# Kernel optimization log

Measured on AMD Instinct MI355X. Metric: run time of the kernel, lower is better.

Reference implementation:

```python
import jax, jax.numpy as jnp
import numpy as np

INITIAL_RADIUS = 1.0  # init_kwargs: initial_radius > 0 -> distance-softmax branch


def reference(xyz, sparse_xyz, sparse_flow, resol_factor, K):
    # xyz: [B,3,N], sparse_xyz: [B,3,M], sparse_flow: [B,3,M]
    q = jnp.transpose(xyz, (0, 2, 1))            # [B,N,3]
    p = jnp.transpose(sparse_xyz, (0, 2, 1))     # [B,M,3]
    flow = jnp.transpose(sparse_flow, (0, 2, 1))  # [B,M,3]

    sigma = INITIAL_RADIUS * resol_factor
    qs = q / sigma
    ps = p / sigma

    # pairwise Euclidean distances [B,N,M]
    sq = (jnp.sum(qs * qs, -1)[:, :, None]
          + jnp.sum(ps * ps, -1)[:, None, :]
          - 2.0 * jnp.einsum('bnc,bmc->bnm', qs, ps))
    dist = jnp.sqrt(jnp.maximum(sq, 1e-12))

    # K nearest: smallest distances
    neg_d, idx = jax.lax.top_k(-dist, K)          # [B,N,K]
    K_dist = -neg_d                               # [B,N,K]

    # gather flow of the K neighbors: [B,N,K,3]
    grouped_flow = jnp.take_along_axis(flow[:, None, :, :], idx[..., None], axis=2)

    # softmax over -distance along K, weighted sum
    K_w = jax.nn.softmax(-K_dist, axis=2)         # [B,N,K]
    dense_flow = jnp.sum(K_w[..., None] * grouped_flow, axis=2)  # [B,N,3]

    return jnp.transpose(dense_flow, (0, 2, 1))   # [B,3,N]


def setup_inputs() -> dict:
    key = jax.random.key(0)
    k1, k2, k3 = jax.random.split(key, 3)
    B, N, M = 4, 16384, 4096
    return {
        'xyz': jax.random.normal(k1, (B, 3, N), dtype=jnp.float32),
        'sparse_xyz': jax.random.normal(k2, (B, 3, M), dtype=jnp.float32),
        'sparse_flow': jax.random.normal(k3, (B, 3, M), dtype=jnp.float32),
        'resol_factor': 1,
        'K': 5,
    }
```

## Files before the change

### kernel.cpp

```cpp
#include <hip/hip_runtime.h>
#include <math.h>
#include <stdint.h>


#define KNN 5
#define SLICES 8
#define BLOCK (SLICES * 64)
#define GRP_SHIFT 8

typedef unsigned int u32;

__device__ __forceinline__ float get_inv_sigma(const int* __restrict__ rf) {
    const int ri = rf[0];
    const float sigma = (ri >= 1 && ri <= 1000000) ? (float)ri : __int_as_float(ri);
    return 1.0f / sigma;
}

__global__ __launch_bounds__(256)
void prep_kernel(const float* __restrict__ sxyz, const int* __restrict__ rf,
                 float4* __restrict__ pts, int M, int total) {
    const int t = blockIdx.x * 256 + threadIdx.x;
    if (t >= total) return;
    const float inv = get_inv_sigma(rf);
    const int b = t / M, m = t - b * M;
    const float* sb = sxyz + (size_t)b * 3 * M;
    const float x = sb[m] * inv;
    const float y = sb[M + m] * inv;
    const float z = sb[2 * M + m] * inv;
    pts[t] = make_float4(x, y, z, fmaf(x, x, fmaf(y, y, z * z)));
}

#define CE_FULL(k, ki, c, ci)                          \
    {                                                  \
        const bool sw = (c) < (k);                     \
        const float vmn = fminf(k, c);                 \
        const float vmx = fmaxf(k, c);                 \
        const u32 nki = sw ? (ci) : (ki);              \
        const u32 nci = sw ? (ki) : (ci);              \
        (k) = vmn; (c) = vmx; (ki) = nki; (ci) = nci;  \
    }
#define CE_LAST(k, ki, c, ci)                          \
    {                                                  \
        const bool sw = (c) < (k);                     \
        (ki) = sw ? (ci) : (ki);                       \
        (k) = fminf(k, c);                             \
    }

template <bool USE_PTS>
__global__ __launch_bounds__(BLOCK, 8)
void knn_kernel(const float* __restrict__ xyz,
                const float* __restrict__ sxyz,
                const float* __restrict__ sflow,
                const int* __restrict__ rf,
                const float4* __restrict__ pts,
                float* __restrict__ out,
                int N, int M) {
    __shared__ float sval_d[SLICES * KNN * 64];
    __shared__ u32   sval_i[SLICES * KNN * 64];

    const int tid  = threadIdx.x;
    const int lane = tid & 63;
    const int wid  = tid >> 6;
    const int swid = __builtin_amdgcn_readfirstlane(wid);
    const int b    = blockIdx.x >> GRP_SHIFT;
    const int grp  = blockIdx.x & ((1 << GRP_SHIFT) - 1);
    const int n    = grp * 64 + lane;

    const float inv = get_inv_sigma(rf);
    const float* qb = xyz + (size_t)b * 3 * N;
    const float qx = qb[n] * inv;
    const float qy = qb[N + n] * inv;
    const float qz = qb[2 * N + n] * inv;
    const float qq = fmaf(qx, qx, fmaf(qy, qy, qz * qz));

    const int CH = M / SLICES;
    const int j0 = swid * CH;

    float e0 = 1e30f, e1 = 1e30f, e2 = 1e30f, e3 = 1e30f, e4 = 1e30f;
    u32   i0 = 0, i1 = 0, i2 = 0, i3 = 0, i4 = 0;

    if constexpr (USE_PTS) {
        const float4* __restrict__ P = pts + (size_t)b * M + j0;
#pragma unroll 4
        for (int j = 0; j < CH; ++j) {
            const float4 p = P[j];
            float t = qx * p.x;
            t = fmaf(qy, p.y, t);
            t = fmaf(qz, p.z, t);
            float c = fmaf(-2.0f, t, p.w);
            u32 ci = (u32)(j0 + j);
            CE_FULL(e0, i0, c, ci)
            CE_FULL(e1, i1, c, ci)
            CE_FULL(e2, i2, c, ci)
            CE_FULL(e3, i3, c, ci)
            CE_LAST(e4, i4, c, ci)
        }
    } else {
        const float* __restrict__ sb = sxyz + (size_t)b * 3 * M;
#pragma unroll 4
        for (int j = 0; j < CH; ++j) {
            const float px = sb[j0 + j] * inv;
            const float py = sb[M + j0 + j] * inv;
            const float pz = sb[2 * M + j0 + j] * inv;
            const float pw = fmaf(px, px, fmaf(py, py, pz * pz));
            float t = qx * px;
            t = fmaf(qy, py, t);
            t = fmaf(qz, pz, t);
            float c = fmaf(-2.0f, t, pw);
            u32 ci = (u32)(j0 + j);
            CE_FULL(e0, i0, c, ci)
            CE_FULL(e1, i1, c, ci)
            CE_FULL(e2, i2, c, ci)
            CE_FULL(e3, i3, c, ci)
            CE_LAST(e4, i4, c, ci)
        }
    }

    sval_d[(wid * KNN + 0) * 64 + lane] = e0;  sval_i[(wid * KNN + 0) * 64 + lane] = i0;
    sval_d[(wid * KNN + 1) * 64 + lane] = e1;  sval_i[(wid * KNN + 1) * 64 + lane] = i1;
    sval_d[(wid * KNN + 2) * 64 + lane] = e2;  sval_i[(wid * KNN + 2) * 64 + lane] = i2;
    sval_d[(wid * KNN + 3) * 64 + lane] = e3;  sval_i[(wid * KNN + 3) * 64 + lane] = i3;
    sval_d[(wid * KNN + 4) * 64 + lane] = e4;  sval_i[(wid * KNN + 4) * 64 + lane] = i4;
    __syncthreads();

    if (wid == 0) {
        float m0 = 1e30f, m1 = 1e30f, m2 = 1e30f, m3 = 1e30f, m4 = 1e30f;
        u32   g0 = 0, g1 = 0, g2 = 0, g3 = 0, g4 = 0;
#pragma unroll
        for (int w = 0; w < SLICES; ++w) {
#pragma unroll
            for (int k = 0; k < KNN; ++k) {
                float c = sval_d[(w * KNN + k) * 64 + lane];
                u32  ci = sval_i[(w * KNN + k) * 64 + lane];
                CE_FULL(m0, g0, c, ci)
                CE_FULL(m1, g1, c, ci)
                CE_FULL(m2, g2, c, ci)
                CE_FULL(m3, g3, c, ci)
                CE_LAST(m4, g4, c, ci)
            }
        }

        const float d0 = sqrtf(fmaxf(m0 + qq, 1e-12f));
        const float d1 = sqrtf(fmaxf(m1 + qq, 1e-12f));
        const float d2 = sqrtf(fmaxf(m2 + qq, 1e-12f));
        const float d3 = sqrtf(fmaxf(m3 + qq, 1e-12f));
        const float d4 = sqrtf(fmaxf(m4 + qq, 1e-12f));
        const float w0 = expf(d0 - d0);
        const float w1 = expf(d0 - d1);
        const float w2 = expf(d0 - d2);
        const float w3 = expf(d0 - d3);
        const float w4 = expf(d0 - d4);
        const float inv_wsum = 1.0f / (w0 + w1 + w2 + w3 + w4);

        const float* fb = sflow + (size_t)b * 3 * M;
        float ax = 0.f, ay = 0.f, az = 0.f;
        ax = fmaf(w0, fb[g0], ax); ay = fmaf(w0, fb[M + g0], ay); az = fmaf(w0, fb[2 * M + g0], az);
        ax = fmaf(w1, fb[g1], ax); ay = fmaf(w1, fb[M + g1], ay); az = fmaf(w1, fb[2 * M + g1], az);
        ax = fmaf(w2, fb[g2], ax); ay = fmaf(w2, fb[M + g2], ay); az = fmaf(w2, fb[2 * M + g2], az);
        ax = fmaf(w3, fb[g3], ax); ay = fmaf(w3, fb[M + g3], ay); az = fmaf(w3, fb[2 * M + g3], az);
        ax = fmaf(w4, fb[g4], ax); ay = fmaf(w4, fb[M + g4], ay); az = fmaf(w4, fb[2 * M + g4], az);

        float* ob = out + (size_t)b * 3 * N;
        ob[n]         = ax * inv_wsum;
        ob[N + n]     = ay * inv_wsum;
        ob[2 * N + n] = az * inv_wsum;
    }
}

extern "C" void kernel_launch(void* const* d_in, const int* in_sizes, int n_in,
                              void* d_out, int out_size, void* d_ws, size_t ws_size,
                              hipStream_t stream) {
    const float* xyz   = (const float*)d_in[0];
    const float* sxyz  = (const float*)d_in[1];
    const float* sflow = (const float*)d_in[2];
    const int*   rf    = (const int*)d_in[3];

    const int B = 4;
    const int N = in_sizes[0] / (3 * B);
    const int M = in_sizes[1] / (3 * B);
    float* out = (float*)d_out;

    const dim3 grid(B * (N / 64));
    const dim3 block(BLOCK);

    const size_t need = (size_t)B * M * sizeof(float4);
    if (ws_size >= need) {
        float4* pts = (float4*)d_ws;
        prep_kernel<<<dim3((B * M + 255) / 256), dim3(256), 0, stream>>>(sxyz, rf, pts, M, B * M);
        knn_kernel<true><<<grid, block, 0, stream>>>(xyz, sxyz, sflow, rf, pts, out, N, M);
    } else {
        knn_kernel<false><<<grid, block, 0, stream>>>(xyz, sxyz, sflow, rf, nullptr, out, N, M);
    }
}
```

Before: 253.0 us.

## Replace brute-force KNN with Morton-ordered uniform grid search plus brute-force tail

Builds a 32^3 uniform grid over the sparse points each call (bbox, histogram, scan, scatter into Morton-ordered cells) and also sorts queries by cell, so each 64-query wavefront covers a compact region. Each wavefront searches cell shells outward, pruning cells whose box distance exceeds the current wave-wide 5th-best distance, instead of scanning all M points. Wavefronts whose query box spans too many cells are queued for a brute-force tail kernel. The cost is many extra small launches, atomics and a memset each call, and search effort that depends on how the data is distributed.

```diff
diff --git a/kernel.cpp b/kernel.cpp
--- a/kernel.cpp
+++ b/kernel.cpp
@@ -4,6 +4,9 @@
 
 
 #define KNN 5
+#define GRID 32
+#define NCELL (GRID * GRID * GRID)
+#define SPAN_TH 128
 #define SLICES 8
 #define BLOCK (SLICES * 64)
 #define GRP_SHIFT 8
@@ -15,6 +18,45 @@
     const float sigma = (ri >= 1 && ri <= 1000000) ? (float)ri : __int_as_float(ri);
     return 1.0f / sigma;
 }
+
+__device__ __forceinline__ float rfl_f(float v) {
+    return __int_as_float(__builtin_amdgcn_readfirstlane(__float_as_int(v)));
+}
+
+__device__ __forceinline__ int cid1(float x, float lo, float ich) {
+    const int c = (int)floorf((x - lo) * ich);
+    return c < 0 ? 0 : (c > GRID - 1 ? GRID - 1 : c);
+}
+
+__device__ __forceinline__ int spread5(int v) {
+    int x = v & 31;
+    x = (x | (x << 8)) & 0x0F00F;
+    x = (x | (x << 4)) & 0x010C3;
+    x = (x | (x << 2)) & 0x01249;
+    return x;
+}
+
+__constant__ int MLUT[32] = {
+    0,    1,    8,    9,    64,   65,   72,   73,   512,  513,  520,
+    521,  576,  577,  584,  585,  4096, 4097, 4104, 4105, 4160, 4161,
+    4168, 4169, 4608, 4609, 4616, 4617, 4672, 4673, 4680, 4681};
+
+#define CE_FULL(k, ki, c, ci)                          \
+    {                                                  \
+        const bool sw = (c) < (k);                     \
+        const float vmn = fminf(k, c);                 \
+        const float vmx = fmaxf(k, c);                 \
+        const u32 nki = sw ? (ci) : (ki);              \
+        const u32 nci = sw ? (ki) : (ci);              \
+        (k) = vmn; (c) = vmx; (ki) = nki; (ci) = nci;  \
+    }
+#define CE_LAST(k, ki, c, ci)                          \
+    {                                                  \
+        const bool sw = (c) < (k);                     \
+        (ki) = sw ? (ci) : (ki);                       \
+        (k) = fminf(k, c);                             \
+    }
+
 
 __global__ __launch_bounds__(256)
 void prep_kernel(const float* __restrict__ sxyz, const int* __restrict__ rf,
@@ -29,22 +71,6 @@
     const float z = sb[2 * M + m] * inv;
     pts[t] = make_float4(x, y, z, fmaf(x, x, fmaf(y, y, z * z)));
 }
-
-#define CE_FULL(k, ki, c, ci)                          \
-    {                                                  \
-        const bool sw = (c) < (k);                     \
-        const float vmn = fminf(k, c);                 \
-        const float vmx = fmaxf(k, c);                 \
-        const u32 nki = sw ? (ci) : (ki);              \
-        const u32 nci = sw ? (ki) : (ci);              \
-        (k) = vmn; (c) = vmx; (ki) = nki; (ci) = nci;  \
-    }
-#define CE_LAST(k, ki, c, ci)                          \
-    {                                                  \
-        const bool sw = (c) < (k);                     \
-        (ki) = sw ? (ci) : (ki);                       \
-        (k) = fminf(k, c);                             \
-    }
 
 template <bool USE_PTS>
 __global__ __launch_bounds__(BLOCK, 8)
@@ -145,7 +171,7 @@
         const float d2 = sqrtf(fmaxf(m2 + qq, 1e-12f));
         const float d3 = sqrtf(fmaxf(m3 + qq, 1e-12f));
         const float d4 = sqrtf(fmaxf(m4 + qq, 1e-12f));
-        const float w0 = expf(d0 - d0);
+        const float w0 = 1.0f;
         const float w1 = expf(d0 - d1);
         const float w2 = expf(d0 - d2);
         const float w3 = expf(d0 - d3);
@@ -167,6 +193,365 @@
     }
 }
 
+
+__global__ __launch_bounds__(256)
+void bbox_kernel(const float* __restrict__ sxyz, const int* __restrict__ rf,
+                 float* __restrict__ bbox, int M) {
+    __shared__ float red[6][256];
+    const int b = blockIdx.x, t = threadIdx.x;
+    const float inv = get_inv_sigma(rf);
+    const float* sb = sxyz + (size_t)b * 3 * M;
+    float lx = 1e30f, ly = 1e30f, lz = 1e30f, hx = -1e30f, hy = -1e30f, hz = -1e30f;
+    for (int m = t; m < M; m += 256) {
+        const float x = sb[m] * inv, y = sb[M + m] * inv, z = sb[2 * M + m] * inv;
+        lx = fminf(lx, x); hx = fmaxf(hx, x);
+        ly = fminf(ly, y); hy = fmaxf(hy, y);
+        lz = fminf(lz, z); hz = fmaxf(hz, z);
+    }
+    red[0][t] = lx; red[1][t] = ly; red[2][t] = lz;
+    red[3][t] = hx; red[4][t] = hy; red[5][t] = hz;
+    __syncthreads();
+    for (int d = 128; d > 0; d >>= 1) {
+        if (t < d) {
+            red[0][t] = fminf(red[0][t], red[0][t + d]);
+            red[1][t] = fminf(red[1][t], red[1][t + d]);
+            red[2][t] = fminf(red[2][t], red[2][t + d]);
+            red[3][t] = fmaxf(red[3][t], red[3][t + d]);
+            red[4][t] = fmaxf(red[4][t], red[4][t + d]);
+            red[5][t] = fmaxf(red[5][t], red[5][t + d]);
+        }
+        __syncthreads();
+    }
+    if (t == 0) {
+        const float sc = (1.0f / GRID) * (1.0f + 4e-6f);
+        bbox[b * 8 + 0] = red[0][0];
+        bbox[b * 8 + 1] = red[1][0];
+        bbox[b * 8 + 2] = red[2][0];
+        bbox[b * 8 + 3] = (red[3][0] - red[0][0]) * sc + 1e-30f;
+        bbox[b * 8 + 4] = (red[4][0] - red[1][0]) * sc + 1e-30f;
+        bbox[b * 8 + 5] = (red[5][0] - red[2][0]) * sc + 1e-30f;
+    }
+}
+
+__global__ __launch_bounds__(256)
+void hist_kernel(const float* __restrict__ src, const int* __restrict__ rf,
+                 const float* __restrict__ bbox, int* __restrict__ hist,
+                 int len, int total) {
+    const int t = blockIdx.x * 256 + threadIdx.x;
+    if (t >= total) return;
+    const int b = t / len, i = t - b * len;
+    const float inv = get_inv_sigma(rf);
+    const float* sb = src + (size_t)b * 3 * len;
+    const float x = sb[i] * inv, y = sb[len + i] * inv, z = sb[2 * len + i] * inv;
+    const float* bb = bbox + b * 8;
+    const int cx = cid1(x, bb[0], 1.0f / bb[3]);
+    const int cy = cid1(y, bb[1], 1.0f / bb[4]);
+    const int cz = cid1(z, bb[2], 1.0f / bb[5]);
+    const int cell = (spread5(cx) << 2) | (spread5(cy) << 1) | spread5(cz);
+    atomicAdd(&hist[(size_t)b * NCELL + cell], 1);
+}
+
+__global__ __launch_bounds__(512)
+void scan_kernel(const int* __restrict__ hist, int* __restrict__ off,
+                 int* __restrict__ cur) {
+    __shared__ int part[512];
+    const int b = blockIdx.x, t = threadIdx.x;
+    const int PER = NCELL / 512;
+    const int hbase = b * NCELL + t * PER;
+    int s = 0;
+    for (int k = 0; k < PER; ++k) s += hist[hbase + k];
+    part[t] = s;
+    __syncthreads();
+    for (int d = 1; d < 512; d <<= 1) {
+        int x = (t >= d) ? part[t - d] : 0;
+        __syncthreads();
+        part[t] += x;
+        __syncthreads();
+    }
+    int run = part[t] - s;
+    const int obase = b * (NCELL + 1) + t * PER;
+    for (int k = 0; k < PER; ++k) {
+        const int h = hist[hbase + k];
+        off[obase + k] = run;
+        cur[hbase + k] = run;
+        run += h;
+    }
+    if (t == 511) off[b * (NCELL + 1) + NCELL] = run;
+}
+
+__global__ __launch_bounds__(256)
+void scatter_kernel(const float* __restrict__ src, const int* __restrict__ rf,
+                    const float* __restrict__ bbox, int* __restrict__ cur,
+                    float4* __restrict__ dst, int* __restrict__ idxDst,
+                    int len, int total, int isQuery) {
+    const int t = blockIdx.x * 256 + threadIdx.x;
+    if (t >= total) return;
+    const int b = t / len, i = t - b * len;
+    const float inv = get_inv_sigma(rf);
+    const float* sb = src + (size_t)b * 3 * len;
+    const float x = sb[i] * inv, y = sb[len + i] * inv, z = sb[2 * len + i] * inv;
+    const float* bb = bbox + b * 8;
+    const int cx = cid1(x, bb[0], 1.0f / bb[3]);
+    const int cy = cid1(y, bb[1], 1.0f / bb[4]);
+    const int cz = cid1(z, bb[2], 1.0f / bb[5]);
+    const int cell = (spread5(cx) << 2) | (spread5(cy) << 1) | spread5(cz);
+    const int slot = atomicAdd(&cur[(size_t)b * NCELL + cell], 1);
+    if (isQuery) {
+        dst[(size_t)b * len + slot] = make_float4(x, y, z, __int_as_float(i));
+    } else {
+        dst[(size_t)b * len + slot] =
+            make_float4(x, y, z, fmaf(x, x, fmaf(y, y, z * z)));
+        idxDst[(size_t)b * len + slot] = i;
+    }
+}
+
+
+#define PROC(CX, CY, CZ)                                                          \
+    {                                                                             \
+        const int cell_ = (MLUT[CX] << 2) | (MLUT[CY] << 1) | MLUT[CZ];           \
+        const int base_ = __builtin_amdgcn_readfirstlane(offb[cell_]);            \
+        const int cnt_ = __builtin_amdgcn_readfirstlane(offb[cell_ + 1]) - base_; \
+        if (cnt_ > 0) {                                                           \
+            const float glx_ = fmaf((float)(CX), chx, lox);                       \
+            const float gly_ = fmaf((float)(CY), chy, loy);                       \
+            const float glz_ = fmaf((float)(CZ), chz, loz);                       \
+            const float dx_ = fmaxf(fmaxf(glx_ - whx, wlx - (glx_ + chx)), 0.0f); \
+            const float dy_ = fmaxf(fmaxf(gly_ - why, wly - (gly_ + chy)), 0.0f); \
+            const float dz_ = fmaxf(fmaxf(glz_ - whz, wlz - (glz_ + chz)), 0.0f); \
+            const float dl_ = fmaf(dx_, dx_, fmaf(dy_, dy_, dz_ * dz_));          \
+            if (!(dl_ > Tw)) {                                                    \
+                for (int j_ = 0; j_ < cnt_; ++j_) {                               \
+                    const float4 p = Pb[base_ + j_];                              \
+                    float t = qx * p.x;                                           \
+                    t = fmaf(qy, p.y, t);                                         \
+                    t = fmaf(qz, p.z, t);                                         \
+                    float c = fmaf(-2.0f, t, p.w);                                \
+                    u32 ci = (u32)(base_ + j_);                                   \
+                    CE_FULL(e0, i0, c, ci)                                        \
+                    CE_FULL(e1, i1, c, ci)                                        \
+                    CE_FULL(e2, i2, c, ci)                                        \
+                    CE_FULL(e3, i3, c, ci)                                        \
+                    CE_LAST(e4, i4, c, ci)                                        \
+                }                                                                 \
+                float m4_ = e4 + qq;                                              \
+                for (int mm_ = 1; mm_ < 64; mm_ <<= 1)                            \
+                    m4_ = fmaxf(m4_, __shfl_xor(m4_, mm_, 64));                   \
+                Tw = rfl_f(m4_);                                                  \
+            }                                                                     \
+        }                                                                         \
+    }
+
+__global__ __launch_bounds__(64)
+void knn_grid_kernel(const float4* __restrict__ qS, const float4* __restrict__ ptsS,
+                     const int* __restrict__ idxS, const int* __restrict__ offC,
+                     const float* __restrict__ bbox, const float* __restrict__ sflow,
+                     int* __restrict__ tailCnt, int* __restrict__ tailList,
+                     float* __restrict__ out, int N, int M) {
+    const int lane = threadIdx.x;
+    const int gpb = N >> 6;
+    const int b = blockIdx.x / gpb;
+    const int grp = blockIdx.x - b * gpb;
+
+    const float4 q4 = qS[(size_t)b * N + grp * 64 + lane];
+    const float qx = q4.x, qy = q4.y, qz = q4.z;
+    const int n = __float_as_int(q4.w);
+    const float qq = fmaf(qx, qx, fmaf(qy, qy, qz * qz));
+
+    float wlx = qx, wly = qy, wlz = qz, whx = qx, why = qy, whz = qz;
+#pragma unroll
+    for (int m = 1; m < 64; m <<= 1) {
+        wlx = fminf(wlx, __shfl_xor(wlx, m, 64));
+        whx = fmaxf(whx, __shfl_xor(whx, m, 64));
+        wly = fminf(wly, __shfl_xor(wly, m, 64));
+        why = fmaxf(why, __shfl_xor(why, m, 64));
+        wlz = fminf(wlz, __shfl_xor(wlz, m, 64));
+        whz = fmaxf(whz, __shfl_xor(whz, m, 64));
+    }
+    const float EPSM = 1e-3f;
+    wlx = rfl_f(wlx) - EPSM; whx = rfl_f(whx) + EPSM;
+    wly = rfl_f(wly) - EPSM; why = rfl_f(why) + EPSM;
+    wlz = rfl_f(wlz) - EPSM; whz = rfl_f(whz) + EPSM;
+
+    const float* bb = bbox + b * 8;
+    const float lox = bb[0], loy = bb[1], loz = bb[2];
+    const float chx = bb[3], chy = bb[4], chz = bb[5];
+    const float hmin = fminf(chx, fminf(chy, chz));
+
+    const int clx = cid1(wlx, lox, 1.0f / chx), cxh = cid1(whx, lox, 1.0f / chx);
+    const int cly = cid1(wly, loy, 1.0f / chy), cyh = cid1(why, loy, 1.0f / chy);
+    const int clz = cid1(wlz, loz, 1.0f / chz), czh = cid1(whz, loz, 1.0f / chz);
+
+    const int span = (cxh - clx + 1) * (cyh - cly + 1) * (czh - clz + 1);
+    if (span > SPAN_TH) {
+        if (lane == 0) {
+            const int idx = atomicAdd(tailCnt, 1);
+            tailList[idx] = blockIdx.x;
+        }
+        return;
+    }
+
+    float e0 = 1e30f, e1 = 1e30f, e2 = 1e30f, e3 = 1e30f, e4 = 1e30f;
+    u32 i0 = 0, i1 = 0, i2 = 0, i3 = 0, i4 = 0;
+    float Tw = 1e30f;
+
+    const float4* __restrict__ Pb = ptsS + (size_t)b * M;
+    const int* __restrict__ offb = offC + (size_t)b * (NCELL + 1);
+
+    for (int r = 0; r <= GRID; ++r) {
+        if (r >= 2) {
+            const float bd = (float)(r - 1) * hmin - EPSM;
+            if (bd > 0.0f && bd * bd > Tw) break;
+        }
+        const int x0 = clx - r < 0 ? 0 : clx - r;
+        const int x1 = cxh + r > GRID - 1 ? GRID - 1 : cxh + r;
+        for (int cx = x0; cx <= x1; ++cx) {
+            const int rx = cx < clx ? clx - cx : (cx > cxh ? cx - cxh : 0);
+            const int y0 = cly - r < 0 ? 0 : cly - r;
+            const int y1 = cyh + r > GRID - 1 ? GRID - 1 : cyh + r;
+            for (int cy = y0; cy <= y1; ++cy) {
+                const int ry = cy < cly ? cly - cy : (cy > cyh ? cy - cyh : 0);
+                const int rxy = rx > ry ? rx : ry;
+                if (rxy == r) {
+                    const int z0 = clz - r < 0 ? 0 : clz - r;
+                    const int z1 = czh + r > GRID - 1 ? GRID - 1 : czh + r;
+                    for (int cz = z0; cz <= z1; ++cz) { PROC(cx, cy, cz) }
+                } else {
+                    int cz = clz - r;
+                    if (cz >= 0) { PROC(cx, cy, cz) }
+                    cz = czh + r;
+                    if (cz <= GRID - 1) { PROC(cx, cy, cz) }
+                }
+            }
+        }
+    }
+
+    const float d0 = sqrtf(fmaxf(e0 + qq, 1e-12f));
+    const float d1 = sqrtf(fmaxf(e1 + qq, 1e-12f));
+    const float d2 = sqrtf(fmaxf(e2 + qq, 1e-12f));
+    const float d3 = sqrtf(fmaxf(e3 + qq, 1e-12f));
+    const float d4 = sqrtf(fmaxf(e4 + qq, 1e-12f));
+    const float w0 = 1.0f;
+    const float w1 = expf(d0 - d1);
+    const float w2 = expf(d0 - d2);
+    const float w3 = expf(d0 - d3);
+    const float w4 = expf(d0 - d4);
+    const float inv_wsum = 1.0f / (w0 + w1 + w2 + w3 + w4);
+
+    const int* __restrict__ idxb = idxS + (size_t)b * M;
+    const int g0 = idxb[i0], g1 = idxb[i1], g2 = idxb[i2], g3 = idxb[i3], g4 = idxb[i4];
+    const float* fb = sflow + (size_t)b * 3 * M;
+    float ax = 0.f, ay = 0.f, az = 0.f;
+    ax = fmaf(w0, fb[g0], ax); ay = fmaf(w0, fb[M + g0], ay); az = fmaf(w0, fb[2 * M + g0], az);
+    ax = fmaf(w1, fb[g1], ax); ay = fmaf(w1, fb[M + g1], ay); az = fmaf(w1, fb[2 * M + g1], az);
+    ax = fmaf(w2, fb[g2], ax); ay = fmaf(w2, fb[M + g2], ay); az = fmaf(w2, fb[2 * M + g2], az);
+    ax = fmaf(w3, fb[g3], ax); ay = fmaf(w3, fb[M + g3], ay); az = fmaf(w3, fb[2 * M + g3], az);
+    ax = fmaf(w4, fb[g4], ax); ay = fmaf(w4, fb[M + g4], ay); az = fmaf(w4, fb[2 * M + g4], az);
+
+    float* ob = out + (size_t)b * 3 * N;
+    ob[n]         = ax * inv_wsum;
+    ob[N + n]     = ay * inv_wsum;
+    ob[2 * N + n] = az * inv_wsum;
+}
+
+__global__ __launch_bounds__(BLOCK, 8)
+void knn_tail_kernel(const float4* __restrict__ qS, const float4* __restrict__ ptsS,
+                     const int* __restrict__ idxS, const int* __restrict__ tailCnt,
+                     const int* __restrict__ tailList, const float* __restrict__ sflow,
+                     float* __restrict__ out, int N, int M) {
+    if ((int)blockIdx.x >= tailCnt[0]) return;
+    const int g = tailList[blockIdx.x];
+    const int gpb = N >> 6;
+    const int b = g / gpb;
+    const int grp = g - b * gpb;
+
+    __shared__ float sval_d[SLICES * KNN * 64];
+    __shared__ u32   sval_i[SLICES * KNN * 64];
+
+    const int tid = threadIdx.x;
+    const int lane = tid & 63;
+    const int wid = tid >> 6;
+    const int swid = __builtin_amdgcn_readfirstlane(wid);
+
+    const float4 q4 = qS[(size_t)b * N + grp * 64 + lane];
+    const float qx = q4.x, qy = q4.y, qz = q4.z;
+    const int n = __float_as_int(q4.w);
+    const float qq = fmaf(qx, qx, fmaf(qy, qy, qz * qz));
+
+    const int CH = M / SLICES;
+    const int j0 = swid * CH;
+
+    float e0 = 1e30f, e1 = 1e30f, e2 = 1e30f, e3 = 1e30f, e4 = 1e30f;
+    u32 i0 = 0, i1 = 0, i2 = 0, i3 = 0, i4 = 0;
+
+    const float4* __restrict__ P = ptsS + (size_t)b * M + j0;
+#pragma unroll 4
+    for (int j = 0; j < CH; ++j) {
+        const float4 p = P[j];
+        float t = qx * p.x;
+        t = fmaf(qy, p.y, t);
+        t = fmaf(qz, p.z, t);
+        float c = fmaf(-2.0f, t, p.w);
+        u32 ci = (u32)(j0 + j);
+        CE_FULL(e0, i0, c, ci)
+        CE_FULL(e1, i1, c, ci)
+        CE_FULL(e2, i2, c, ci)
+        CE_FULL(e3, i3, c, ci)
+        CE_LAST(e4, i4, c, ci)
+    }
+
+    sval_d[(wid * KNN + 0) * 64 + lane] = e0;  sval_i[(wid * KNN + 0) * 64 + lane] = i0;
+    sval_d[(wid * KNN + 1) * 64 + lane] = e1;  sval_i[(wid * KNN + 1) * 64 + lane] = i1;
+    sval_d[(wid * KNN + 2) * 64 + lane] = e2;  sval_i[(wid * KNN + 2) * 64 + lane] = i2;
+    sval_d[(wid * KNN + 3) * 64 + lane] = e3;  sval_i[(wid * KNN + 3) * 64 + lane] = i3;
+    sval_d[(wid * KNN + 4) * 64 + lane] = e4;  sval_i[(wid * KNN + 4) * 64 + lane] = i4;
+    __syncthreads();
+
+    if (wid == 0) {
+        float m0 = 1e30f, m1 = 1e30f, m2 = 1e30f, m3 = 1e30f, m4 = 1e30f;
+        u32 g0 = 0, g1 = 0, g2 = 0, g3 = 0, g4 = 0;
+#pragma unroll
+        for (int w = 0; w < SLICES; ++w) {
+#pragma unroll
+            for (int k = 0; k < KNN; ++k) {
+                float c = sval_d[(w * KNN + k) * 64 + lane];
+                u32 ci = sval_i[(w * KNN + k) * 64 + lane];
+                CE_FULL(m0, g0, c, ci)
+                CE_FULL(m1, g1, c, ci)
+                CE_FULL(m2, g2, c, ci)
+                CE_FULL(m3, g3, c, ci)
+                CE_LAST(m4, g4, c, ci)
+            }
+        }
+
+        const float d0 = sqrtf(fmaxf(m0 + qq, 1e-12f));
+        const float d1 = sqrtf(fmaxf(m1 + qq, 1e-12f));
+        const float d2 = sqrtf(fmaxf(m2 + qq, 1e-12f));
+        const float d3 = sqrtf(fmaxf(m3 + qq, 1e-12f));
+        const float d4 = sqrtf(fmaxf(m4 + qq, 1e-12f));
+        const float w0 = 1.0f;
+        const float w1 = expf(d0 - d1);
+        const float w2 = expf(d0 - d2);
+        const float w3 = expf(d0 - d3);
+        const float w4 = expf(d0 - d4);
+        const float inv_wsum = 1.0f / (w0 + w1 + w2 + w3 + w4);
+
+        const int* __restrict__ idxb = idxS + (size_t)b * M;
+        const int o0 = idxb[g0], o1 = idxb[g1], o2 = idxb[g2], o3 = idxb[g3], o4 = idxb[g4];
+        const float* fb = sflow + (size_t)b * 3 * M;
+        float ax = 0.f, ay = 0.f, az = 0.f;
+        ax = fmaf(w0, fb[o0], ax); ay = fmaf(w0, fb[M + o0], ay); az = fmaf(w0, fb[2 * M + o0], az);
+        ax = fmaf(w1, fb[o1], ax); ay = fmaf(w1, fb[M + o1], ay); az = fmaf(w1, fb[2 * M + o1], az);
+        ax = fmaf(w2, fb[o2], ax); ay = fmaf(w2, fb[M + o2], ay); az = fmaf(w2, fb[2 * M + o2], az);
+        ax = fmaf(w3, fb[o3], ax); ay = fmaf(w3, fb[M + o3], ay); az = fmaf(w3, fb[2 * M + o3], az);
+        ax = fmaf(w4, fb[o4], ax); ay = fmaf(w4, fb[M + o4], ay); az = fmaf(w4, fb[2 * M + o4], az);
+
+        float* ob = out + (size_t)b * 3 * N;
+        ob[n]         = ax * inv_wsum;
+        ob[N + n]     = ay * inv_wsum;
+        ob[2 * N + n] = az * inv_wsum;
+    }
+}
+
 extern "C" void kernel_launch(void* const* d_in, const int* in_sizes, int n_in,
                               void* d_out, int out_size, void* d_ws, size_t ws_size,
                               hipStream_t stream) {
@@ -179,16 +564,51 @@
     const int N = in_sizes[0] / (3 * B);
     const int M = in_sizes[1] / (3 * B);
     float* out = (float*)d_out;
-
-    const dim3 grid(B * (N / 64));
-    const dim3 block(BLOCK);
-
-    const size_t need = (size_t)B * M * sizeof(float4);
-    if (ws_size >= need) {
-        float4* pts = (float4*)d_ws;
-        prep_kernel<<<dim3((B * M + 255) / 256), dim3(256), 0, stream>>>(sxyz, rf, pts, M, B * M);
-        knn_kernel<true><<<grid, block, 0, stream>>>(xyz, sxyz, sflow, rf, pts, out, N, M);
+    const int gpb = N / 64;
+
+    size_t o = 0;
+    float4* ptsS = (float4*)((char*)d_ws + o); o += (size_t)B * M * sizeof(float4);
+    float4* qS   = (float4*)((char*)d_ws + o); o += (size_t)B * N * sizeof(float4);
+    int* idxS    = (int*)((char*)d_ws + o);    o += (size_t)B * M * 4;
+    float* bbox  = (float*)((char*)d_ws + o);  o += 256;
+    int* histC   = (int*)((char*)d_ws + o);    o += (size_t)B * NCELL * 4;
+    int* histQ   = (int*)((char*)d_ws + o);    o += (size_t)B * NCELL * 4;
+    int* tailCnt = (int*)((char*)d_ws + o);    o += 64;
+    int* tailList= (int*)((char*)d_ws + o);    o += (size_t)B * gpb * 4;
+    int* offC    = (int*)((char*)d_ws + o);    o += (size_t)B * (NCELL + 1) * 4;
+    int* offQ    = (int*)((char*)d_ws + o);    o += (size_t)B * (NCELL + 1) * 4;
+    int* curC    = (int*)((char*)d_ws + o);    o += (size_t)B * NCELL * 4;
+    int* curQ    = (int*)((char*)d_ws + o);    o += (size_t)B * NCELL * 4;
+    const size_t need = o;
+
+    if (ws_size >= need && (N % 64) == 0 && (M % SLICES) == 0) {
+        bbox_kernel<<<dim3(B), dim3(256), 0, stream>>>(sxyz, rf, bbox, M);
+        hipMemsetAsync(histC, 0, (size_t)B * NCELL * 8 + 64, stream);
+        hist_kernel<<<dim3((B * M + 255) / 256), dim3(256), 0, stream>>>(
+            sxyz, rf, bbox, histC, M, B * M);
+        hist_kernel<<<dim3((B * N + 255) / 256), dim3(256), 0, stream>>>(
+            xyz, rf, bbox, histQ, N, B * N);
+        scan_kernel<<<dim3(B), dim3(512), 0, stream>>>(histC, offC, curC);
+        scan_kernel<<<dim3(B), dim3(512), 0, stream>>>(histQ, offQ, curQ);
+        scatter_kernel<<<dim3((B * M + 255) / 256), dim3(256), 0, stream>>>(
+            sxyz, rf, bbox, curC, ptsS, idxS, M, B * M, 0);
+        scatter_kernel<<<dim3((B * N + 255) / 256), dim3(256), 0, stream>>>(
+            xyz, rf, bbox, curQ, qS, idxS, N, B * N, 1);
+        knn_grid_kernel<<<dim3(B * gpb), dim3(64), 0, stream>>>(
+            qS, ptsS, idxS, offC, bbox, sflow, tailCnt, tailList, out, N, M);
+        knn_tail_kernel<<<dim3(B * gpb), dim3(BLOCK), 0, stream>>>(
+            qS, ptsS, idxS, tailCnt, tailList, sflow, out, N, M);
     } else {
-        knn_kernel<false><<<grid, block, 0, stream>>>(xyz, sxyz, sflow, rf, nullptr, out, N, M);
-    }
-}
+        const dim3 grid(B * (N / 64));
+        const dim3 block(BLOCK);
+        const size_t needOld = (size_t)B * M * sizeof(float4);
+        if (ws_size >= needOld) {
+            float4* pts = (float4*)d_ws;
+            prep_kernel<<<dim3((B * M + 255) / 256), dim3(256), 0, stream>>>(
+                sxyz, rf, pts, M, B * M);
+            knn_kernel<true><<<grid, block, 0, stream>>>(xyz, sxyz, sflow, rf, pts, out, N, M);
+        } else {
+            knn_kernel<false><<<grid, block, 0, stream>>>(xyz, sxyz, sflow, rf, nullptr, out, N, M);
+        }
+    }
+}
```

After: 773.5 us. 3.06x slower.
